# Performance work log

Measured on AMD Instinct MI355X. Metric: run time of the kernel, lower is better.

The kernel has to match this reference:

```python
import jax, jax.numpy as jnp
import numpy as np

C = 128          # hidden_channels
H = 8            # num_heads
D = C // H       # head dim = 16
OUT = 64         # out_channels
L = 2            # num_layers
NN = (30000, 60000, 6000)                 # poi, road, region node counts
NE = (200000, 300000, 200000, 100000)     # edges per edge type
ETS = ((0, 1), (1, 1), (1, 2), (2, 0))    # (src_type, dst_type) per edge type


def setup_inputs():
    key = jax.random.key(0)
    ks = iter(jax.random.split(key, 40))
    s = 1.0 / np.sqrt(C)
    sd = 1.0 / np.sqrt(D)
    inp = {}
    inp['x_poi'] = jax.random.normal(next(ks), (NN[0], C), jnp.float32)
    inp['x_road'] = jax.random.normal(next(ks), (NN[1], C), jnp.float32)
    inp['x_region'] = jax.random.normal(next(ks), (NN[2], C), jnp.float32)
    for et, (si, di) in enumerate(ETS):
        inp[f'e{et}_src'] = jax.random.randint(next(ks), (NE[et],), 0, NN[si], jnp.int32)
        inp[f'e{et}_dst'] = jax.random.randint(next(ks), (NE[et],), 0, NN[di], jnp.int32)
    # per-node-type input projection
    inp['lin_w'] = jax.random.normal(next(ks), (3, C, C), jnp.float32) * s
    inp['lin_b'] = jax.random.normal(next(ks), (3, C), jnp.float32) * 0.01
    # per-layer, per-node-type K/Q/V and output projections
    for nm in ('kw', 'qw', 'vw', 'aw'):
        inp[nm] = jax.random.normal(next(ks), (L, 3, C, C), jnp.float32) * s
    for nm in ('kb', 'qb', 'vb', 'ab'):
        inp[nm] = jax.random.normal(next(ks), (L, 3, C), jnp.float32) * 0.01
    # per-layer, per-edge-type relation matrices and priors
    inp['a_rel'] = jax.random.normal(next(ks), (L, 4, H, D, D), jnp.float32) * sd
    inp['m_rel'] = jax.random.normal(next(ks), (L, 4, H, D, D), jnp.float32) * sd
    inp['p_rel'] = jnp.ones((L, 4, H), jnp.float32)
    inp['skip'] = jnp.ones((L, 3), jnp.float32)
    inp['out_w'] = jax.random.normal(next(ks), (C, OUT), jnp.float32) * s
    inp['out_b'] = jnp.zeros((OUT,), jnp.float32)
    return inp


def _seg_softmax(alpha, dst, n):
    amax = jax.lax.stop_gradient(jax.ops.segment_max(alpha, dst, num_segments=n))
    ex = jnp.exp(alpha - amax[dst])
    den = jax.ops.segment_sum(ex, dst, num_segments=n)
    return ex / (den[dst] + 1e-16)


def _hgt_forward(xs, edges, lin_w, lin_b, kw, kb, qw, qb, vw, vb, aw, ab,
                 a_rel, m_rel, p_rel, skip, out_w, out_b):
    # per-node-type input linear + relu
    xs = [jax.nn.relu(xs[i] @ lin_w[i] + lin_b[i]) for i in range(3)]
    scale = 1.0 / np.sqrt(D)
    for l in range(L):
        k = [(xs[i] @ kw[l, i] + kb[l, i]).reshape(-1, H, D) for i in range(3)]
        q = [(xs[i] @ qw[l, i] + qb[l, i]).reshape(-1, H, D) for i in range(3)]
        v = [(xs[i] @ vw[l, i] + vb[l, i]).reshape(-1, H, D) for i in range(3)]
        agg = [jnp.zeros((NN[i], H, D), xs[i].dtype) for i in range(3)]
        for et, (si, di) in enumerate(ETS):
            src, dst = edges[et]
            n = NN[di]
            ke = jnp.einsum('ehd,hdf->ehf', k[si][src], a_rel[l, et])   # [E,H,D]
            alpha = jnp.einsum('ehd,ehd->eh', q[di][dst], ke) * p_rel[l, et] * scale
            alpha = _seg_softmax(alpha, dst, n)                          # [E,H]
            m = jnp.einsum('ehd,hdf->ehf', v[si][src], m_rel[l, et])    # [E,H,D]
            agg[di] = agg[di] + jax.ops.segment_sum(m * alpha[..., None], dst, num_segments=n)
        new_xs = []
        for i in range(3):
            o = jax.nn.gelu(agg[i].reshape(-1, C)) @ aw[l, i] + ab[l, i]
            beta = jax.nn.sigmoid(skip[l, i])
            o = beta * o + (1.0 - beta) * xs[i]
            new_xs.append(jax.nn.relu(o))  # HGT applies activation after each conv
        xs = new_xs
    return (xs[0] @ out_w + out_b, xs[1] @ out_w + out_b, xs[2] @ out_w + out_b)


def reference(x_poi, x_road, x_region,
              e0_src, e0_dst, e1_src, e1_dst, e2_src, e2_dst, e3_src, e3_dst,
              lin_w, lin_b, kw, kb, qw, qb, vw, vb, aw, ab,
              a_rel, m_rel, p_rel, skip, out_w, out_b):
    edges = ((e0_src, e0_dst), (e1_src, e1_dst), (e2_src, e2_dst), (e3_src, e3_dst))
    return _hgt_forward([x_poi, x_road, x_region], edges,
                        lin_w, lin_b, kw, kb, qw, qb, vw, vb, aw, ab,
                        a_rel, m_rel, p_rel, skip, out_w, out_b)
```

## Files before the change

### kernel.cpp

```cpp
#include <hip/hip_runtime.h>
#include <cstddef>
#include <cstdint>


typedef __attribute__((ext_vector_type(8))) short short8;
typedef __attribute__((ext_vector_type(4))) float floatx4;

__device__ __forceinline__ float gelu_fast(float x) {
    float u = 1.5957691216057308f * x * (1.0f + 0.044715f * x * x);
    return x / (1.0f + __expf(-u));
}

__device__ __forceinline__ unsigned short f2bf(float f) {
    unsigned u = __float_as_uint(f);
    u += 0x7fffu + ((u >> 16) & 1);
    return (unsigned short)(u >> 16);
}

__device__ __forceinline__ float bf2f(unsigned short h) {
    return __uint_as_float((unsigned)h << 16);
}

__device__ __forceinline__ void up8(uint4 u, float* f) {
    f[0] = __uint_as_float(u.x << 16); f[1] = __uint_as_float(u.x & 0xffff0000u);
    f[2] = __uint_as_float(u.y << 16); f[3] = __uint_as_float(u.y & 0xffff0000u);
    f[4] = __uint_as_float(u.z << 16); f[5] = __uint_as_float(u.z & 0xffff0000u);
    f[6] = __uint_as_float(u.w << 16); f[7] = __uint_as_float(u.w & 0xffff0000u);
}

__device__ __forceinline__ uint4 pk8(const float* f) {
    uint4 u;
    u.x = (unsigned)f2bf(f[0]) | ((unsigned)f2bf(f[1]) << 16);
    u.y = (unsigned)f2bf(f[2]) | ((unsigned)f2bf(f[3]) << 16);
    u.z = (unsigned)f2bf(f[4]) | ((unsigned)f2bf(f[5]) << 16);
    u.w = (unsigned)f2bf(f[6]) | ((unsigned)f2bf(f[7]) << 16);
    return u;
}

__global__ __launch_bounds__(256, 2) void gemm_proj_all(
    const unsigned short* __restrict__ xs_bf,
    const unsigned short* __restrict__ Wl,
    const float* __restrict__ bl,
    unsigned short* __restrict__ proj)
{
    const int    NN_[3]  = {30000, 60000, 6000};
    const int    NPAN[3] = {469, 938, 94};
    const int    OFFr[3] = {0, 30000, 90000};
    const int    WOFF[3] = {0, 49152, 131072};
    const int    BOFF[3] = {0, 384, 1024};
    const size_t POFF[3] = {0, 11520000u, 49920000u};
    const int    LDO[3]  = {384, 640, 384};

    int b = blockIdx.x, t, cp, rb;
    if (b < 590)      { t = 1; cp = b / 118; rb = b - cp * 118; }
    else if (b < 767) { int lb = b - 590; t = 0; cp = lb / 59; rb = lb - cp * 59; }
    else              { int lb = b - 767; t = 2; cp = lb / 12; rb = lb - cp * 12; }
    int p0 = rb * 8, p1 = p0 + 8;
    if (p1 > NPAN[t]) p1 = NPAN[t];

    const unsigned short* Abf = xs_bf + (size_t)OFFr[t] * 128;
    const unsigned short* Wt  = Wl + WOFF[t];
    const float* bias = bl + BOFF[t] + cp * 128;
    unsigned short* outbf = proj + POFF[t];
    const int ldo = LDO[t], Nrows = NN_[t];

    const int wave = threadIdx.x >> 6, lane = threadIdx.x & 63;
    const int quad = lane >> 4, l16 = lane & 15;

    short8 B[2][4][4];
    {
        const unsigned short* wb = Wt + (size_t)(cp * 128 + l16) * 128 + quad * 8;
        #pragma unroll
        for (int T = 0; T < 2; ++T)
            #pragma unroll
            for (int c = 0; c < 4; ++c)
                #pragma unroll
                for (int kc = 0; kc < 4; ++kc)
                    B[T][c][kc] = *(const short8*)(wb + (size_t)(T * 64 + c * 16) * 128 + kc * 32);
    }
    float4 bv[2][4];
    #pragma unroll
    for (int T = 0; T < 2; ++T)
        #pragma unroll
        for (int c = 0; c < 4; ++c)
            bv[T][c] = *(const float4*)(bias + T * 64 + c * 16 + quad * 4);

    short8 Acur[4];
    {
        int m = p0 * 64 + wave * 16 + l16; if (m >= Nrows) m = Nrows - 1;
        const unsigned short* ap = Abf + (size_t)m * 128 + quad * 8;
        #pragma unroll
        for (int kc = 0; kc < 4; ++kc) Acur[kc] = *(const short8*)(ap + kc * 32);
    }
    for (int p = p0; p < p1; ++p) {
        short8 Anx[4];
        {
            int m = (p + 1) * 64 + wave * 16 + l16; if (m >= Nrows) m = Nrows - 1;
            const unsigned short* ap = Abf + (size_t)m * 128 + quad * 8;
            #pragma unroll
            for (int kc = 0; kc < 4; ++kc) Anx[kc] = *(const short8*)(ap + kc * 32);
        }
        floatx4 acc[2][4];
        #pragma unroll
        for (int T = 0; T < 2; ++T)
            #pragma unroll
            for (int c = 0; c < 4; ++c) acc[T][c] = (floatx4){0.f, 0.f, 0.f, 0.f};
        #pragma unroll
        for (int kc = 0; kc < 4; ++kc)
            #pragma unroll
            for (int T = 0; T < 2; ++T)
                #pragma unroll
                for (int c = 0; c < 4; ++c)
                    acc[T][c] = __builtin_amdgcn_mfma_f32_16x16x32_bf16(B[T][c][kc], Acur[kc], acc[T][c], 0, 0, 0);
        int node = p * 64 + wave * 16 + l16;
        if (node < Nrows) {
            unsigned short* op = outbf + (size_t)node * ldo + cp * 128 + quad * 4;
            #pragma unroll
            for (int T = 0; T < 2; ++T)
                #pragma unroll
                for (int c = 0; c < 4; ++c) {
                    uint2 u;
                    u.x = (unsigned)f2bf(acc[T][c][0] + bv[T][c].x) |
                          ((unsigned)f2bf(acc[T][c][1] + bv[T][c].y) << 16);
                    u.y = (unsigned)f2bf(acc[T][c][2] + bv[T][c].z) |
                          ((unsigned)f2bf(acc[T][c][3] + bv[T][c].w) << 16);
                    *(uint2*)(op + T * 64 + c * 16) = u;
                }
        }
        #pragma unroll
        for (int kc = 0; kc < 4; ++kc) Acur[kc] = Anx[kc];
    }
}

template<bool AF32, bool GIN, bool SKIP>
__global__ __launch_bounds__(256, 2) void gemm_node(
    const void* __restrict__ a0v, const void* __restrict__ a1v, const void* __restrict__ a2v,
    const unsigned short* __restrict__ WtB, const float* __restrict__ biasB,
    const unsigned short* __restrict__ xoldB, const float* __restrict__ skipB,
    unsigned short* __restrict__ outB)
{
    const int TN[3]   = {30000, 60000, 6000};
    const int NPAN[3] = {469, 938, 94};
    const int TOFF[3] = {0, 30000, 90000};
    int b = blockIdx.x, t, rb;
    if (b < 235)      { t = 0; rb = b; }
    else if (b < 704) { t = 1; rb = b - 235; }
    else              { t = 2; rb = b - 704; }
    int p0 = rb * 2, p1 = p0 + 2;
    if (p1 > NPAN[t]) p1 = NPAN[t];
    int Nrows = TN[t];
    const void* av = (t == 0) ? a0v : (t == 1) ? a1v : a2v;
    const unsigned short* xold = xoldB + (size_t)TOFF[t] * 128;
    unsigned short* out = outB + (size_t)TOFF[t] * 128;

    const int wave = threadIdx.x >> 6, lane = threadIdx.x & 63;
    const int quad = lane >> 4, l16 = lane & 15;

    short8 B[8][4];
    {
        const unsigned short* wb = WtB + (size_t)t * 16384 + (size_t)l16 * 128 + quad * 8;
        #pragma unroll
        for (int c = 0; c < 8; ++c)
            #pragma unroll
            for (int kc = 0; kc < 4; ++kc)
                B[c][kc] = *(const short8*)(wb + (size_t)c * 2048 + kc * 32);
    }
    float beta = 0.f, omb = 0.f;
    if (SKIP) { beta = 1.0f / (1.0f + __expf(-skipB[t])); omb = 1.0f - beta; }

    short8 Acur[4];
    {
        int m = p0 * 64 + wave * 16 + l16; if (m >= Nrows) m = Nrows - 1;
        size_t base = (size_t)m * 128 + quad * 8;
        #pragma unroll
        for (int kc = 0; kc < 4; ++kc) {
            if (AF32) {
                const float* ap = (const float*)av + base;
                float4 f0 = *(const float4*)(ap + kc * 32);
                float4 f1 = *(const float4*)(ap + kc * 32 + 4);
                float af[8] = {f0.x, f0.y, f0.z, f0.w, f1.x, f1.y, f1.z, f1.w};
                short8 a;
                #pragma unroll
                for (int i = 0; i < 8; ++i) a[i] = (short)f2bf(af[i]);
                Acur[kc] = a;
            } else if (GIN) {
                const unsigned short* ap = (const unsigned short*)av + base;
                short8 a8 = *(const short8*)(ap + kc * 32);
                short8 a;
                #pragma unroll
                for (int i = 0; i < 8; ++i)
                    a[i] = (short)f2bf(gelu_fast(bf2f((unsigned short)a8[i])));
                Acur[kc] = a;
            } else {
                const unsigned short* ap = (const unsigned short*)av + base;
                Acur[kc] = *(const short8*)(ap + kc * 32);
            }
        }
    }
    for (int p = p0; p < p1; ++p) {
        float4 Fnx[4][2];
        short8 Snx[4];
        {
            int m = (p + 1) * 64 + wave * 16 + l16; if (m >= Nrows) m = Nrows - 1;
            size_t base = (size_t)m * 128 + quad * 8;
            #pragma unroll
            for (int kc = 0; kc < 4; ++kc) {
                if (AF32) {
                    const float* ap = (const float*)av + base;
                    Fnx[kc][0] = *(const float4*)(ap + kc * 32);
                    Fnx[kc][1] = *(const float4*)(ap + kc * 32 + 4);
                } else {
                    const unsigned short* ap = (const unsigned short*)av + base;
                    Snx[kc] = *(const short8*)(ap + kc * 32);
                }
            }
        }
        int node = p * 64 + wave * 16 + l16;
        int ncl = (node < Nrows) ? node : (Nrows - 1);
        uint2 xo[8];
        if (SKIP) {
            #pragma unroll
            for (int c = 0; c < 8; ++c)
                xo[c] = *(const uint2*)(xold + (size_t)ncl * 128 + c * 16 + quad * 4);
        }
        floatx4 acc[8];
        #pragma unroll
        for (int c = 0; c < 8; ++c) acc[c] = (floatx4){0.f, 0.f, 0.f, 0.f};
        #pragma unroll
        for (int kc = 0; kc < 4; ++kc)
            #pragma unroll
            for (int c = 0; c < 8; ++c)
                acc[c] = __builtin_amdgcn_mfma_f32_16x16x32_bf16(B[c][kc], Acur[kc], acc[c], 0, 0, 0);
        if (node < Nrows) {
            #pragma unroll
            for (int c = 0; c < 8; ++c) {
                int col0 = c * 16 + quad * 4;
                float4 bv = *(const float4*)(biasB + t * 128 + col0);
                float o0 = acc[c][0] + bv.x, o1 = acc[c][1] + bv.y;
                float o2 = acc[c][2] + bv.z, o3 = acc[c][3] + bv.w;
                if (SKIP) {
                    o0 = beta * o0 + omb * __uint_as_float(xo[c].x << 16);
                    o1 = beta * o1 + omb * __uint_as_float(xo[c].x & 0xffff0000u);
                    o2 = beta * o2 + omb * __uint_as_float(xo[c].y << 16);
                    o3 = beta * o3 + omb * __uint_as_float(xo[c].y & 0xffff0000u);
                }
                o0 = fmaxf(o0, 0.f); o1 = fmaxf(o1, 0.f);
                o2 = fmaxf(o2, 0.f); o3 = fmaxf(o3, 0.f);
                uint2 u;
                u.x = (unsigned)f2bf(o0) | ((unsigned)f2bf(o1) << 16);
                u.y = (unsigned)f2bf(o2) | ((unsigned)f2bf(o3) << 16);
                *(uint2*)(out + (size_t)node * 128 + col0) = u;
            }
        }
        #pragma unroll
        for (int kc = 0; kc < 4; ++kc) {
            if (AF32) {
                float af[8] = {Fnx[kc][0].x, Fnx[kc][0].y, Fnx[kc][0].z, Fnx[kc][0].w,
                               Fnx[kc][1].x, Fnx[kc][1].y, Fnx[kc][1].z, Fnx[kc][1].w};
                short8 a;
                #pragma unroll
                for (int i = 0; i < 8; ++i) a[i] = (short)f2bf(af[i]);
                Acur[kc] = a;
            } else if (GIN) {
                short8 a;
                #pragma unroll
                for (int i = 0; i < 8; ++i)
                    a[i] = (short)f2bf(gelu_fast(bf2f((unsigned short)Snx[kc][i])));
                Acur[kc] = a;
            } else {
                Acur[kc] = Snx[kc];
            }
        }
    }
}

__global__ __launch_bounds__(256, 3) void gemm_out(
    const unsigned short* __restrict__ Abf,
    const unsigned short* __restrict__ Wt,
    const float* __restrict__ bias,
    float* __restrict__ out, int Nrows)
{
    const int wave = threadIdx.x >> 6, lane = threadIdx.x & 63;
    const int quad = lane >> 4, l16 = lane & 15;
    int p0 = blockIdx.x * 4, p1 = p0 + 4;

    short8 B[4][4];
    {
        const unsigned short* wb = Wt + (size_t)l16 * 128 + quad * 8;
        #pragma unroll
        for (int c = 0; c < 4; ++c)
            #pragma unroll
            for (int kc = 0; kc < 4; ++kc)
                B[c][kc] = *(const short8*)(wb + (size_t)c * 2048 + kc * 32);
    }
    float4 bv[4];
    #pragma unroll
    for (int c = 0; c < 4; ++c) bv[c] = *(const float4*)(bias + c * 16 + quad * 4);

    short8 Acur[4];
    {
        int m = p0 * 64 + wave * 16 + l16; if (m >= Nrows) m = Nrows - 1;
        const unsigned short* ap = Abf + (size_t)m * 128 + quad * 8;
        #pragma unroll
        for (int kc = 0; kc < 4; ++kc) Acur[kc] = *(const short8*)(ap + kc * 32);
    }
    for (int p = p0; p < p1; ++p) {
        short8 Anx[4];
        {
            int m = (p + 1) * 64 + wave * 16 + l16; if (m >= Nrows) m = Nrows - 1;
            const unsigned short* ap = Abf + (size_t)m * 128 + quad * 8;
            #pragma unroll
            for (int kc = 0; kc < 4; ++kc) Anx[kc] = *(const short8*)(ap + kc * 32);
        }
        floatx4 acc[4];
        #pragma unroll
        for (int c = 0; c < 4; ++c) acc[c] = (floatx4){0.f, 0.f, 0.f, 0.f};
        #pragma unroll
        for (int kc = 0; kc < 4; ++kc)
            #pragma unroll
            for (int c = 0; c < 4; ++c)
                acc[c] = __builtin_amdgcn_mfma_f32_16x16x32_bf16(B[c][kc], Acur[kc], acc[c], 0, 0, 0);
        int node = p * 64 + wave * 16 + l16;
        if (node < Nrows) {
            #pragma unroll
            for (int c = 0; c < 4; ++c) {
                float4 o;
                o.x = acc[c][0] + bv[c].x; o.y = acc[c][1] + bv[c].y;
                o.z = acc[c][2] + bv[c].z; o.w = acc[c][3] + bv[c].w;
                *(float4*)(out + (size_t)node * 64 + c * 16 + quad * 4) = o;
            }
        }
        #pragma unroll
        for (int kc = 0; kc < 4; ++kc) Acur[kc] = Anx[kc];
    }
}

__global__ __launch_bounds__(128) void prep_qpack(
    const float* __restrict__ qw, const float* __restrict__ qb,
    unsigned short* __restrict__ Wpack, float* __restrict__ bpack)
{
    const int pre[3] = {0, 49152, 131072};
    const int preB[3] = {0, 384, 1024};
    int n = threadIdx.x, k = blockIdx.x, t = blockIdx.y, l = blockIdx.z;
    unsigned short* Wp = Wpack + (size_t)l * 180224 + pre[t];
    Wp[(size_t)n * 128 + k] = f2bf(qw[(size_t)(l * 3 + t) * 16384 + (size_t)k * 128 + n]);
    if (k == 0) bpack[l * 1408 + preB[t] + n] = qb[(l * 3 + t) * 128 + n];
}

__global__ __launch_bounds__(128) void fold_rel_pack(
    const float* __restrict__ kw, const float* __restrict__ kb,
    const float* __restrict__ vw, const float* __restrict__ vb,
    const float* __restrict__ a_rel, const float* __restrict__ m_rel,
    unsigned short* __restrict__ Wpack, float* __restrict__ bpack)
{
    const int SIv[4] = {0, 1, 1, 2};
    const int SLOT[4] = {0, 0, 1, 0};
    const int pre[3] = {0, 49152, 131072};
    const int preB[3] = {0, 384, 1024};
    int hf = threadIdx.x, h = hf >> 4, f = hf & 15;
    int c = blockIdx.x, et = blockIdx.y, l = blockIdx.z;
    int si = SIv[et];
    const float* kwp  = kw + (size_t)(l * 3 + si) * 16384;
    const float* vwp  = vw + (size_t)(l * 3 + si) * 16384;
    const float* kbp  = kb + (size_t)(l * 3 + si) * 128;
    const float* vbp  = vb + (size_t)(l * 3 + si) * 128;
    const float* arel = a_rel + (size_t)(l * 4 + et) * 2048;
    const float* mrel = m_rel + (size_t)(l * 4 + et) * 2048;
    float sk = 0.f, sv = 0.f;
    #pragma unroll
    for (int d = 0; d < 16; ++d) {
        float ar = arel[(h * 16 + d) * 16 + f];
        float mr = mrel[(h * 16 + d) * 16 + f];
        sk = fmaf(kwp[c * 128 + h * 16 + d], ar, sk);
        sv = fmaf(vwp[c * 128 + h * 16 + d], mr, sv);
    }
    int rowoff = 128 + 256 * SLOT[et];
    unsigned short* Wp = Wpack + (size_t)l * 180224 + pre[si];
    Wp[(size_t)(rowoff + hf) * 128 + c]       = f2bf(sk);
    Wp[(size_t)(rowoff + 128 + hf) * 128 + c] = f2bf(sv);
    if (c == 0) {
        float bk = 0.f, bvv = 0.f;
        #pragma unroll
        for (int d = 0; d < 16; ++d) {
            bk  = fmaf(kbp[h * 16 + d], arel[(h * 16 + d) * 16 + f], bk);
            bvv = fmaf(vbp[h * 16 + d], mrel[(h * 16 + d) * 16 + f], bvv);
        }
        float* bp = bpack + l * 1408 + preB[si];
        bp[rowoff + hf]       = bk;
        bp[rowoff + 128 + hf] = bvv;
    }
}

__global__ __launch_bounds__(128) void prep_w9(
    const float* __restrict__ lin_w, const float* __restrict__ aw,
    unsigned short* __restrict__ lwt, unsigned short* __restrict__ awt)
{
    int n = threadIdx.x, k = blockIdx.x, mi = blockIdx.y;
    const float* w; unsigned short* wt; int m;
    if (mi < 3) { w = lin_w; wt = lwt; m = mi; }
    else        { w = aw;    wt = awt; m = mi - 3; }
    wt[(size_t)m * 16384 + (size_t)n * 128 + k] =
        f2bf(w[(size_t)m * 16384 + (size_t)k * 128 + n]);
}

__global__ __launch_bounds__(64) void prep_owt(
    const float* __restrict__ ow, unsigned short* __restrict__ owt)
{
    int n = threadIdx.x, k = blockIdx.x;
    owt[(size_t)n * 128 + k] = f2bf(ow[(size_t)k * 64 + n]);
}

__global__ __launch_bounds__(256) void hist_all(
    const int* __restrict__ d0, const int* __restrict__ d1,
    const int* __restrict__ d2, const int* __restrict__ d3,
    int* __restrict__ deg4)
{
    const int Ev[4] = {200000, 300000, 200000, 100000};
    int et = blockIdx.y;
    int e = blockIdx.x * 256 + threadIdx.x;
    if (e >= Ev[et]) return;
    const int* d = et == 0 ? d0 : et == 1 ? d1 : et == 2 ? d2 : d3;
    atomicAdd(&deg4[et * 60000 + d[e]], 1);
}

__global__ __launch_bounds__(256) void scan_tile_all(
    const int* __restrict__ deg4,
    int* __restrict__ r0, int* __restrict__ r1, int* __restrict__ r2, int* __restrict__ r3,
    int* __restrict__ tsum4)
{
    const int Ndv[4] = {60000, 60000, 6000, 30000};
    __shared__ int ls[256];
    int et = blockIdx.y;
    int n = Ndv[et];
    const int* deg = deg4 + et * 60000;
    int* rowptr = et == 0 ? r0 : et == 1 ? r1 : et == 2 ? r2 : r3;
    int b = blockIdx.x, tid = threadIdx.x;
    int base = b * 1024 + tid * 4;
    int v0 = 0, v1 = 0, v2 = 0, v3 = 0;
    if (base + 3 < n) {
        int4 t = *(const int4*)(deg + base);
        v0 = t.x; v1 = t.y; v2 = t.z; v3 = t.w;
    } else {
        if (base + 0 < n) v0 = deg[base + 0];
        if (base + 1 < n) v1 = deg[base + 1];
        if (base + 2 < n) v2 = deg[base + 2];
        if (base + 3 < n) v3 = deg[base + 3];
    }
    int s = v0 + v1 + v2 + v3;
    ls[tid] = s;
    __syncthreads();
    #pragma unroll
    for (int off = 1; off < 256; off <<= 1) {
        int t = (tid >= off) ? ls[tid - off] : 0;
        __syncthreads();
        ls[tid] += t;
        __syncthreads();
    }
    int run = ls[tid] - s;
    int o0 = run; run += v0;
    int o1 = run; run += v1;
    int o2 = run; run += v2;
    int o3 = run;
    if (base + 3 < n) {
        *(int4*)(rowptr + base) = make_int4(o0, o1, o2, o3);
    } else {
        if (base + 0 < n) rowptr[base + 0] = o0;
        if (base + 1 < n) rowptr[base + 1] = o1;
        if (base + 2 < n) rowptr[base + 2] = o2;
    }
    if (tid == 255) tsum4[et * 64 + b] = ls[255];
}

__global__ __launch_bounds__(64) void scan_tsum_all(
    int* __restrict__ tsum4,
    int* __restrict__ r0, int* __restrict__ r1, int* __restrict__ r2, int* __restrict__ r3)
{
    const int Ndv[4] = {60000, 60000, 6000, 30000};
    int et = blockIdx.x;
    int n = Ndv[et];
    int nt = (n + 1023) >> 10;
    int* tileSum = tsum4 + et * 64;
    int* rowptr = et == 0 ? r0 : et == 1 ? r1 : et == 2 ? r2 : r3;
    int tid = threadIdx.x;
    int v = (tid < nt) ? tileSum[tid] : 0;
    int orig = v;
    #pragma unroll
    for (int off = 1; off < 64; off <<= 1) {
        int t = __shfl_up(v, off);
        if (tid >= off) v += t;
    }
    if (tid < nt) tileSum[tid] = v - orig;
    if (tid == nt - 1) rowptr[n] = v;
}

__global__ __launch_bounds__(256) void scan_add_all(
    int* __restrict__ r0, int* __restrict__ r1, int* __restrict__ r2, int* __restrict__ r3,
    const int* __restrict__ tsum4)
{
    const int Ndv[4] = {60000, 60000, 6000, 30000};
    int et = blockIdx.y;
    int n = Ndv[et];
    int* rowptr = et == 0 ? r0 : et == 1 ? r1 : et == 2 ? r2 : r3;
    int i = blockIdx.x * 256 + threadIdx.x;
    if (i < n) rowptr[i] += tsum4[et * 64 + (i >> 10)];
}

__global__ __launch_bounds__(256) void fill_all(
    const int* __restrict__ s0, const int* __restrict__ d0,
    const int* __restrict__ s1, const int* __restrict__ d1,
    const int* __restrict__ s2, const int* __restrict__ d2,
    const int* __restrict__ s3, const int* __restrict__ d3,
    const int* __restrict__ r0, const int* __restrict__ r1,
    const int* __restrict__ r2, const int* __restrict__ r3,
    int* __restrict__ deg4,
    int* __restrict__ c0, int* __restrict__ c1, int* __restrict__ c2, int* __restrict__ c3)
{
    const int Ev[4] = {200000, 300000, 200000, 100000};
    int et = blockIdx.y;
    int e = blockIdx.x * 256 + threadIdx.x;
    if (e >= Ev[et]) return;
    const int* src = et == 0 ? s0 : et == 1 ? s1 : et == 2 ? s2 : s3;
    const int* dst = et == 0 ? d0 : et == 1 ? d1 : et == 2 ? d2 : d3;
    const int* rowptr = et == 0 ? r0 : et == 1 ? r1 : et == 2 ? r2 : r3;
    int* csr = et == 0 ? c0 : et == 1 ? c1 : et == 2 ? c2 : c3;
    int d = dst[e];
    int pos = atomicAdd(&deg4[et * 60000 + d], 1);
    csr[rowptr[d] + pos] = src[e];
}

__device__ __forceinline__ int perm_key(
    const int* rp0, const int* rp1, const int* rp2, const int* rp3,
    int sec, int i)
{
    int d;
    if (sec == 0)      d = (rp0[i + 1] - rp0[i]) + (rp1[i + 1] - rp1[i]);
    else if (sec == 1) d = rp3[i + 1] - rp3[i];
    else               d = rp2[i + 1] - rp2[i];
    return d < 511 ? d : 511;
}

__global__ __launch_bounds__(256) void perm_hist(
    const int* __restrict__ rp0, const int* __restrict__ rp1,
    const int* __restrict__ rp2, const int* __restrict__ rp3,
    int* __restrict__ hist)
{
    const int N[3] = {60000, 30000, 6000};
    __shared__ int lh[512];
    int sec = blockIdx.y, tid = threadIdx.x;
    lh[tid] = 0; lh[tid + 256] = 0;
    __syncthreads();
    int i = blockIdx.x * 256 + tid;
    if (i < N[sec])
        atomicAdd(&lh[perm_key(rp0, rp1, rp2, rp3, sec, i)], 1);
    __syncthreads();
    if (lh[tid])       atomicAdd(&hist[sec * 512 + tid],       lh[tid]);
    if (lh[tid + 256]) atomicAdd(&hist[sec * 512 + tid + 256], lh[tid + 256]);
}

__global__ __launch_bounds__(512) void perm_scan(int* __restrict__ hist)
{
    __shared__ int ls[512];
    int* h = hist + blockIdx.x * 512;
    int tid = threadIdx.x;
    int v = h[tid];
    ls[tid] = v;
    __syncthreads();
    for (int off = 1; off < 512; off <<= 1) {
        int t = (tid >= off) ? ls[tid - off] : 0;
        __syncthreads();
        ls[tid] += t;
        __syncthreads();
    }
    h[tid] = ls[tid] - v;
}

__global__ __launch_bounds__(256) void perm_scatter(
    const int* __restrict__ rp0, const int* __restrict__ rp1,
    const int* __restrict__ rp2, const int* __restrict__ rp3,
    int* __restrict__ hist,
    int* __restrict__ permR, int* __restrict__ permP, int* __restrict__ permG)
{
    const int N[3] = {60000, 30000, 6000};
    __shared__ int lh[512];
    __shared__ int lofs[512];
    int sec = blockIdx.y, tid = threadIdx.x;
    lh[tid] = 0; lh[tid + 256] = 0;
    __syncthreads();
    int i = blockIdx.x * 256 + tid;
    int d = -1, lrank = 0;
    if (i < N[sec]) {
        d = perm_key(rp0, rp1, rp2, rp3, sec, i);
        lrank = atomicAdd(&lh[d], 1);
    }
    __syncthreads();
    if (lh[tid])       lofs[tid]       = atomicAdd(&hist[sec * 512 + tid],       lh[tid]);
    if (lh[tid + 256]) lofs[tid + 256] = atomicAdd(&hist[sec * 512 + tid + 256], lh[tid + 256]);
    __syncthreads();
    if (i < N[sec]) {
        int* perm = (sec == 0) ? permR : (sec == 1) ? permP : permG;
        perm[lofs[d] + lrank] = i;
    }
}

__device__ __forceinline__ void attn_edge(
    uint4 k0, uint4 k1, uint4 v0, uint4 v1,
    const float* qf, float ph, float& m, float& l, float* o)
{
    float kf[16];
    up8(k0, kf); up8(k1, kf + 8);
    float a = 0.f;
    #pragma unroll
    for (int i = 0; i < 16; ++i) a = fmaf(qf[i], kf[i], a);
    a *= ph;
    float d = a - m;
    if (d > 8.f) {
        float sc = __expf(-d);
        l *= sc;
        #pragma unroll
        for (int i = 0; i < 16; ++i) o[i] *= sc;
        m = a; d = 0.f;
    }
    float w = __expf(d);
    l += w;
    float vf[16];
    up8(v0, vf); up8(v1, vf + 8);
    #pragma unroll
    for (int i = 0; i < 16; ++i) o[i] = fmaf(w, vf[i], o[i]);
}

__device__ __forceinline__ void attn_run(
    const int* __restrict__ csr, int beg, int end,
    const unsigned short* __restrict__ kbase, int ld,
    const float* qf, float ph, float& m, float& l, float* o)
{
    int n = end - beg;
    if (n <= 0) return;
    const uint4* pA = (const uint4*)(kbase + (size_t)csr[beg] * ld);
    uint4 A0 = pA[0], A1 = pA[1], A2 = pA[16], A3 = pA[17];
    uint4 B0 = A0, B1 = A1, B2 = A2, B3 = A3;
    if (n > 1) {
        const uint4* pB = (const uint4*)(kbase + (size_t)csr[beg + 1] * ld);
        B0 = pB[0]; B1 = pB[1]; B2 = pB[16]; B3 = pB[17];
    }
    int j = beg;
    for (; j + 3 < end; j += 2) {
        const uint4* pC = (const uint4*)(kbase + (size_t)csr[j + 2] * ld);
        const uint4* pD = (const uint4*)(kbase + (size_t)csr[j + 3] * ld);
        uint4 C0 = pC[0], C1 = pC[1], C2 = pC[16], C3 = pC[17];
        uint4 D0 = pD[0], D1 = pD[1], D2 = pD[16], D3 = pD[17];
        float kf0[16], kf1[16];
        up8(A0, kf0); up8(A1, kf0 + 8);
        up8(B0, kf1); up8(B1, kf1 + 8);
        float a0 = 0.f, a1 = 0.f;
        #pragma unroll
        for (int i = 0; i < 16; ++i) {
            a0 = fmaf(qf[i], kf0[i], a0);
            a1 = fmaf(qf[i], kf1[i], a1);
        }
        a0 *= ph; a1 *= ph;
        float hi = fmaxf(a0, a1);
        float d = hi - m;
        if (d > 8.f) {
            float sc = __expf(-d);
            l *= sc;
            #pragma unroll
            for (int i = 0; i < 16; ++i) o[i] *= sc;
            m = hi;
        }
        float w0 = __expf(a0 - m), w1 = __expf(a1 - m);
        l += w0 + w1;
        float vf0[16], vf1[16];
        up8(A2, vf0); up8(A3, vf0 + 8);
        up8(B2, vf1); up8(B3, vf1 + 8);
        #pragma unroll
        for (int i = 0; i < 16; ++i)
            o[i] = fmaf(w1, vf1[i], fmaf(w0, vf0[i], o[i]));
        A0 = C0; A1 = C1; A2 = C2; A3 = C3;
        B0 = D0; B1 = D1; B2 = D2; B3 = D3;
    }
    int rem = end - j;
    attn_edge(A0, A1, A2, A3, qf, ph, m, l, o);
    if (rem >= 2) attn_edge(B0, B1, B2, B3, qf, ph, m, l, o);
    if (rem == 3) {
        const uint4* pC = (const uint4*)(kbase + (size_t)csr[j + 2] * ld);
        attn_edge(pC[0], pC[1], pC[16], pC[17], qf, ph, m, l, o);
    }
}

__global__ __launch_bounds__(256) void agg_all(
    const int* __restrict__ rp0, const int* __restrict__ cs0,
    const int* __restrict__ rp1, const int* __restrict__ cs1,
    const int* __restrict__ rp2, const int* __restrict__ cs2,
    const int* __restrict__ rp3, const int* __restrict__ cs3,
    const unsigned short* __restrict__ P0, const unsigned short* __restrict__ P1,
    const unsigned short* __restrict__ P2,
    const float* __restrict__ prl,
    const int* __restrict__ pmR, const int* __restrict__ pmP,
    const int* __restrict__ pmG,
    unsigned short* __restrict__ num)
{
    int gb = blockIdx.x, tid = threadIdx.x;
    float qf[16], o[16], r[16];
    if (gb < 1875) {
        int t = gb * 256 + tid;
        int node = pmR[t >> 3], h = t & 7;
        const uint4* qp = (const uint4*)(P1 + (size_t)node * 640 + h * 16);
        up8(qp[0], qf); up8(qp[1], qf + 8);
        float m0 = -INFINITY, l0 = 0.f;
        #pragma unroll
        for (int i = 0; i < 16; ++i) o[i] = 0.f;
        attn_run(cs0, rp0[node], rp0[node + 1], P0 + 128 + h * 16, 384,
                 qf, prl[h] * 0.25f, m0, l0, o);
        float i0 = 1.f / (l0 + 1e-16f);
        #pragma unroll
        for (int i = 0; i < 16; ++i) { r[i] = i0 * o[i]; o[i] = 0.f; }
        float m1 = -INFINITY, l1 = 0.f;
        attn_run(cs1, rp1[node], rp1[node + 1], P1 + 128 + h * 16, 640,
                 qf, prl[8 + h] * 0.25f, m1, l1, o);
        float i1 = 1.f / (l1 + 1e-16f);
        #pragma unroll
        for (int i = 0; i < 16; ++i) r[i] += i1 * o[i];
        uint4* np = (uint4*)(num + (size_t)(30000 + node) * 128 + h * 16);
        np[0] = pk8(r); np[1] = pk8(r + 8);
    } else if (gb < 2625) {
        int t = (gb - 1875) * 256 + tid;
        int node = pmG[t >> 5], h = t & 7, sub = (t >> 3) & 3;
        int beg0 = rp2[node], end0 = rp2[node + 1];
        int n = end0 - beg0;
        int beg = beg0 + ((n * sub) >> 2);
        int end = beg0 + ((n * (sub + 1)) >> 2);
        const uint4* qp = (const uint4*)(P2 + (size_t)node * 384 + h * 16);
        up8(qp[0], qf); up8(qp[1], qf + 8);
        float m = -INFINITY, l = 0.f;
        #pragma unroll
        for (int i = 0; i < 16; ++i) o[i] = 0.f;
        attn_run(cs2, beg, end, P1 + 384 + h * 16, 640,
                 qf, prl[16 + h] * 0.25f, m, l, o);
        #pragma unroll
        for (int st = 8; st <= 16; st <<= 1) {
            float mp = __shfl_xor(m, st);
            float lp = __shfl_xor(l, st);
            float mn = fmaxf(m, mp);
            float sc  = (l  > 0.f) ? __expf(m  - mn) : 0.f;
            float scp = (lp > 0.f) ? __expf(mp - mn) : 0.f;
            l = l * sc + lp * scp;
            #pragma unroll
            for (int i = 0; i < 16; ++i) {
                float op = __shfl_xor(o[i], st);
                o[i] = o[i] * sc + op * scp;
            }
            m = mn;
        }
        if (sub) return;
        float inv = 1.f / (l + 1e-16f);
        #pragma unroll
        for (int i = 0; i < 16; ++i) r[i] = inv * o[i];
        uint4* np = (uint4*)(num + (size_t)(90000 + node) * 128 + h * 16);
        np[0] = pk8(r); np[1] = pk8(r + 8);
    } else {
        int t = (gb - 2625) * 256 + tid;
        if (t >= 240000) return;
        int node = pmP[t >> 3], h = t & 7;
        const uint4* qp = (const uint4*)(P0 + (size_t)node * 384 + h * 16);
        up8(qp[0], qf); up8(qp[1], qf + 8);
        float m = -INFINITY, l = 0.f;
        #pragma unroll
        for (int i = 0; i < 16; ++i) o[i] = 0.f;
        attn_run(cs3, rp3[node], rp3[node + 1], P2 + 128 + h * 16, 384,
                 qf, prl[24 + h] * 0.25f, m, l, o);
        float inv = 1.f / (l + 1e-16f);
        #pragma unroll
        for (int i = 0; i < 16; ++i) r[i] = inv * o[i];
        uint4* np = (uint4*)(num + (size_t)node * 128 + h * 16);
        np[0] = pk8(r); np[1] = pk8(r + 8);
    }
}

extern "C" void kernel_launch(void* const* d_in, const int* in_sizes, int n_in,
                              void* d_out, int out_size, void* d_ws, size_t ws_size,
                              hipStream_t stream)
{
    (void)in_sizes; (void)n_in; (void)out_size; (void)ws_size;

    const float* xin[3] = {(const float*)d_in[0], (const float*)d_in[1], (const float*)d_in[2]};
    const int* esrc[4] = {(const int*)d_in[3], (const int*)d_in[5], (const int*)d_in[7], (const int*)d_in[9]};
    const int* edst[4] = {(const int*)d_in[4], (const int*)d_in[6], (const int*)d_in[8], (const int*)d_in[10]};
    const float* lin_w = (const float*)d_in[11];
    const float* lin_b = (const float*)d_in[12];
    const float* kw = (const float*)d_in[13];
    const float* qw = (const float*)d_in[14];
    const float* vw = (const float*)d_in[15];
    const float* aw = (const float*)d_in[16];
    const float* kb = (const float*)d_in[17];
    const float* qb = (const float*)d_in[18];
    const float* vb = (const float*)d_in[19];
    const float* ab = (const float*)d_in[20];
    const float* a_rel = (const float*)d_in[21];
    const float* m_rel = (const float*)d_in[22];
    const float* p_rel = (const float*)d_in[23];
    const float* skip  = (const float*)d_in[24];
    const float* out_w = (const float*)d_in[25];
    const float* out_b = (const float*)d_in[26];

    float* ws = (float*)d_ws;
    unsigned short* num   = (unsigned short*)ws;
    unsigned short* xs_bf = (unsigned short*)(ws + 6144000);
    unsigned short* proj  = (unsigned short*)(ws + 12288000);
    unsigned short* Wpack = (unsigned short*)(ws + 38400000);
    unsigned short* lwt   = (unsigned short*)(ws + 38580224);
    unsigned short* awt   = (unsigned short*)(ws + 38604800);
    unsigned short* owt   = (unsigned short*)(ws + 38653952);
    float*          bpack = ws + 38658048;
    int*            deg4  = (int*)(ws + 38660864);
    int*            tsum4 = (int*)(ws + 38900864);
    int* rp[4];
    rp[0] = (int*)(ws + 38901120);
    rp[1] = (int*)(ws + 38961128);
    rp[2] = (int*)(ws + 39021136);
    rp[3] = (int*)(ws + 39027144);
    int* cs[4];
    cs[0] = (int*)(ws + 39057152);
    cs[1] = (int*)(ws + 39257152);
    cs[2] = (int*)(ws + 39557152);
    cs[3] = (int*)(ws + 39757152);
    int* permR = deg4;
    int* permP = deg4 + 60000;
    int* permG = deg4 + 90000;
    int* phist = deg4 + 96000;

    unsigned short* P[3];
    P[0] = proj;
    P[1] = proj + (size_t)30000 * 384;
    P[2] = proj + (size_t)30000 * 384 + (size_t)60000 * 640;

    dim3 blk(256);

    hipMemsetAsync(deg4, 0, 960000, stream);
    hist_all<<<dim3(1172, 4), blk, 0, stream>>>(edst[0], edst[1], edst[2], edst[3], deg4);
    scan_tile_all<<<dim3(59, 4), blk, 0, stream>>>(deg4, rp[0], rp[1], rp[2], rp[3], tsum4);
    scan_tsum_all<<<dim3(4), dim3(64), 0, stream>>>(tsum4, rp[0], rp[1], rp[2], rp[3]);
    scan_add_all<<<dim3(235, 4), blk, 0, stream>>>(rp[0], rp[1], rp[2], rp[3], tsum4);
    hipMemsetAsync(deg4, 0, 960000, stream);
    fill_all<<<dim3(1172, 4), blk, 0, stream>>>(
        esrc[0], edst[0], esrc[1], edst[1], esrc[2], edst[2], esrc[3], edst[3],
        rp[0], rp[1], rp[2], rp[3], deg4, cs[0], cs[1], cs[2], cs[3]);

    hipMemsetAsync(phist, 0, 1536 * 4, stream);
    perm_hist<<<dim3(235, 3), blk, 0, stream>>>(rp[0], rp[1], rp[2], rp[3], phist);
    perm_scan<<<dim3(3), dim3(512), 0, stream>>>(phist);
    perm_scatter<<<dim3(235, 3), blk, 0, stream>>>(
        rp[0], rp[1], rp[2], rp[3], phist, permR, permP, permG);

    prep_qpack<<<dim3(128, 3, 2), dim3(128), 0, stream>>>(qw, qb, Wpack, bpack);
    fold_rel_pack<<<dim3(128, 4, 2), dim3(128), 0, stream>>>(
        kw, kb, vw, vb, a_rel, m_rel, Wpack, bpack);
    prep_w9<<<dim3(128, 9), dim3(128), 0, stream>>>(lin_w, aw, lwt, awt);
    prep_owt<<<dim3(128), dim3(64), 0, stream>>>(out_w, owt);

    gemm_node<true, false, false><<<dim3(751), blk, 0, stream>>>(
        xin[0], xin[1], xin[2], lwt, lin_b, nullptr, nullptr, xs_bf);

    for (int l = 0; l < 2; ++l) {
        gemm_proj_all<<<dim3(803), blk, 0, stream>>>(
            xs_bf, Wpack + (size_t)l * 180224, bpack + l * 1408, proj);

        agg_all<<<dim3(3563), blk, 0, stream>>>(
            rp[0], cs[0], rp[1], cs[1], rp[2], cs[2], rp[3], cs[3],
            P[0], P[1], P[2], p_rel + (size_t)l * 32,
            permR, permP, permG, num);

        gemm_node<false, true, true><<<dim3(751), blk, 0, stream>>>(
            num, num + (size_t)30000 * 128, num + (size_t)90000 * 128,
            awt + (size_t)l * 3 * 16384, ab + (size_t)l * 3 * 128,
            xs_bf, skip + l * 3, xs_bf);
    }

    gemm_out<<<dim3(375), blk, 0, stream>>>(
        xs_bf, owt, out_b, (float*)d_out, 96000);
}
```

Before: 589.9 us.

## Split road and POI attention edges across two lanes, fuse prep kernels

```diff
diff --git a/kernel.cpp b/kernel.cpp
--- a/kernel.cpp
+++ b/kernel.cpp
@@ -335,79 +335,74 @@
     }
 }
 
-__global__ __launch_bounds__(128) void prep_qpack(
+__global__ __launch_bounds__(128) void prep_all(
     const float* __restrict__ qw, const float* __restrict__ qb,
-    unsigned short* __restrict__ Wpack, float* __restrict__ bpack)
-{
-    const int pre[3] = {0, 49152, 131072};
-    const int preB[3] = {0, 384, 1024};
-    int n = threadIdx.x, k = blockIdx.x, t = blockIdx.y, l = blockIdx.z;
-    unsigned short* Wp = Wpack + (size_t)l * 180224 + pre[t];
-    Wp[(size_t)n * 128 + k] = f2bf(qw[(size_t)(l * 3 + t) * 16384 + (size_t)k * 128 + n]);
-    if (k == 0) bpack[l * 1408 + preB[t] + n] = qb[(l * 3 + t) * 128 + n];
-}
-
-__global__ __launch_bounds__(128) void fold_rel_pack(
     const float* __restrict__ kw, const float* __restrict__ kb,
     const float* __restrict__ vw, const float* __restrict__ vb,
     const float* __restrict__ a_rel, const float* __restrict__ m_rel,
-    unsigned short* __restrict__ Wpack, float* __restrict__ bpack)
-{
-    const int SIv[4] = {0, 1, 1, 2};
-    const int SLOT[4] = {0, 0, 1, 0};
+    const float* __restrict__ lin_w, const float* __restrict__ aw,
+    const float* __restrict__ ow,
+    unsigned short* __restrict__ Wpack, float* __restrict__ bpack,
+    unsigned short* __restrict__ lwt, unsigned short* __restrict__ awt,
+    unsigned short* __restrict__ owt)
+{
     const int pre[3] = {0, 49152, 131072};
     const int preB[3] = {0, 384, 1024};
-    int hf = threadIdx.x, h = hf >> 4, f = hf & 15;
-    int c = blockIdx.x, et = blockIdx.y, l = blockIdx.z;
-    int si = SIv[et];
-    const float* kwp  = kw + (size_t)(l * 3 + si) * 16384;
-    const float* vwp  = vw + (size_t)(l * 3 + si) * 16384;
-    const float* kbp  = kb + (size_t)(l * 3 + si) * 128;
-    const float* vbp  = vb + (size_t)(l * 3 + si) * 128;
-    const float* arel = a_rel + (size_t)(l * 4 + et) * 2048;
-    const float* mrel = m_rel + (size_t)(l * 4 + et) * 2048;
-    float sk = 0.f, sv = 0.f;
-    #pragma unroll
-    for (int d = 0; d < 16; ++d) {
-        float ar = arel[(h * 16 + d) * 16 + f];
-        float mr = mrel[(h * 16 + d) * 16 + f];
-        sk = fmaf(kwp[c * 128 + h * 16 + d], ar, sk);
-        sv = fmaf(vwp[c * 128 + h * 16 + d], mr, sv);
-    }
-    int rowoff = 128 + 256 * SLOT[et];
-    unsigned short* Wp = Wpack + (size_t)l * 180224 + pre[si];
-    Wp[(size_t)(rowoff + hf) * 128 + c]       = f2bf(sk);
-    Wp[(size_t)(rowoff + 128 + hf) * 128 + c] = f2bf(sv);
-    if (c == 0) {
-        float bk = 0.f, bvv = 0.f;
+    int b = blockIdx.x;
+    if (b < 768) {
+        int n = threadIdx.x;
+        int k = b & 127, r = b >> 7, t = r % 3, l = r / 3;
+        unsigned short* Wp = Wpack + (size_t)l * 180224 + pre[t];
+        Wp[(size_t)n * 128 + k] = f2bf(qw[(size_t)(l * 3 + t) * 16384 + (size_t)k * 128 + n]);
+        if (k == 0) bpack[l * 1408 + preB[t] + n] = qb[(l * 3 + t) * 128 + n];
+    } else if (b < 1792) {
+        const int SIv[4] = {0, 1, 1, 2};
+        const int SLOT[4] = {0, 0, 1, 0};
+        int bb = b - 768;
+        int hf = threadIdx.x, h = hf >> 4, f = hf & 15;
+        int c = bb & 127, et = (bb >> 7) & 3, l = bb >> 9;
+        int si = SIv[et];
+        const float* kwp  = kw + (size_t)(l * 3 + si) * 16384;
+        const float* vwp  = vw + (size_t)(l * 3 + si) * 16384;
+        const float* kbp  = kb + (size_t)(l * 3 + si) * 128;
+        const float* vbp  = vb + (size_t)(l * 3 + si) * 128;
+        const float* arel = a_rel + (size_t)(l * 4 + et) * 2048;
+        const float* mrel = m_rel + (size_t)(l * 4 + et) * 2048;
+        float sk = 0.f, sv = 0.f;
         #pragma unroll
         for (int d = 0; d < 16; ++d) {
-            bk  = fmaf(kbp[h * 16 + d], arel[(h * 16 + d) * 16 + f], bk);
-            bvv = fmaf(vbp[h * 16 + d], mrel[(h * 16 + d) * 16 + f], bvv);
-        }
-        float* bp = bpack + l * 1408 + preB[si];
-        bp[rowoff + hf]       = bk;
-        bp[rowoff + 128 + hf] = bvv;
-    }
-}
-
-__global__ __launch_bounds__(128) void prep_w9(
-    const float* __restrict__ lin_w, const float* __restrict__ aw,
-    unsigned short* __restrict__ lwt, unsigned short* __restrict__ awt)
-{
-    int n = threadIdx.x, k = blockIdx.x, mi = blockIdx.y;
-    const float* w; unsigned short* wt; int m;
-    if (mi < 3) { w = lin_w; wt = lwt; m = mi; }
-    else        { w = aw;    wt = awt; m = mi - 3; }
-    wt[(size_t)m * 16384 + (size_t)n * 128 + k] =
-        f2bf(w[(size_t)m * 16384 + (size_t)k * 128 + n]);
-}
-
-__global__ __launch_bounds__(64) void prep_owt(
-    const float* __restrict__ ow, unsigned short* __restrict__ owt)
-{
-    int n = threadIdx.x, k = blockIdx.x;
-    owt[(size_t)n * 128 + k] = f2bf(ow[(size_t)k * 64 + n]);
+            float ar = arel[(h * 16 + d) * 16 + f];
+            float mr = mrel[(h * 16 + d) * 16 + f];
+            sk = fmaf(kwp[c * 128 + h * 16 + d], ar, sk);
+            sv = fmaf(vwp[c * 128 + h * 16 + d], mr, sv);
+        }
+        int rowoff = 128 + 256 * SLOT[et];
+        unsigned short* Wp = Wpack + (size_t)l * 180224 + pre[si];
+        Wp[(size_t)(rowoff + hf) * 128 + c]       = f2bf(sk);
+        Wp[(size_t)(rowoff + 128 + hf) * 128 + c] = f2bf(sv);
+        if (c == 0) {
+            float bk = 0.f, bvv = 0.f;
+            #pragma unroll
+            for (int d = 0; d < 16; ++d) {
+                bk  = fmaf(kbp[h * 16 + d], arel[(h * 16 + d) * 16 + f], bk);
+                bvv = fmaf(vbp[h * 16 + d], mrel[(h * 16 + d) * 16 + f], bvv);
+            }
+            float* bp = bpack + l * 1408 + preB[si];
+            bp[rowoff + hf]       = bk;
+            bp[rowoff + 128 + hf] = bvv;
+        }
+    } else if (b < 2944) {
+        int bb = b - 1792;
+        int n = threadIdx.x, k = bb & 127, mi = bb >> 7;
+        const float* w; unsigned short* wt; int m;
+        if (mi < 3) { w = lin_w; wt = lwt; m = mi; }
+        else        { w = aw;    wt = awt; m = mi - 3; }
+        wt[(size_t)m * 16384 + (size_t)n * 128 + k] =
+            f2bf(w[(size_t)m * 16384 + (size_t)k * 128 + n]);
+    } else {
+        int k = b - 2944, n = threadIdx.x;
+        if (n < 64) owt[(size_t)n * 128 + k] = f2bf(ow[(size_t)k * 64 + n]);
+    }
 }
 
 __global__ __launch_bounds__(256) void hist_all(
@@ -687,6 +682,22 @@
     }
 }
 
+__device__ __forceinline__ void merge_sm(float& m, float& l, float* o, int st)
+{
+    float mp = __shfl_xor(m, st);
+    float lp = __shfl_xor(l, st);
+    float mn = fmaxf(m, mp);
+    float sc  = (l  > 0.f) ? __expf(m  - mn) : 0.f;
+    float scp = (lp > 0.f) ? __expf(mp - mn) : 0.f;
+    l = l * sc + lp * scp;
+    #pragma unroll
+    for (int i = 0; i < 16; ++i) {
+        float op = __shfl_xor(o[i], st);
+        o[i] = o[i] * sc + op * scp;
+    }
+    m = mn;
+}
+
 __global__ __launch_bounds__(256) void agg_all(
     const int* __restrict__ rp0, const int* __restrict__ cs0,
     const int* __restrict__ rp1, const int* __restrict__ cs1,
@@ -701,30 +712,37 @@
 {
     int gb = blockIdx.x, tid = threadIdx.x;
     float qf[16], o[16], r[16];
-    if (gb < 1875) {
+    if (gb < 3750) {
         int t = gb * 256 + tid;
-        int node = pmR[t >> 3], h = t & 7;
+        int node = pmR[59999 - (t >> 4)], h = t & 7, half = (t >> 3) & 1;
         const uint4* qp = (const uint4*)(P1 + (size_t)node * 640 + h * 16);
         up8(qp[0], qf); up8(qp[1], qf + 8);
+        int beg = rp0[node], end = rp0[node + 1], n = end - beg;
+        int b0 = beg + ((n * half) >> 1), e0 = beg + ((n * (half + 1)) >> 1);
         float m0 = -INFINITY, l0 = 0.f;
         #pragma unroll
         for (int i = 0; i < 16; ++i) o[i] = 0.f;
-        attn_run(cs0, rp0[node], rp0[node + 1], P0 + 128 + h * 16, 384,
+        attn_run(cs0, b0, e0, P0 + 128 + h * 16, 384,
                  qf, prl[h] * 0.25f, m0, l0, o);
+        merge_sm(m0, l0, o, 8);
         float i0 = 1.f / (l0 + 1e-16f);
         #pragma unroll
         for (int i = 0; i < 16; ++i) { r[i] = i0 * o[i]; o[i] = 0.f; }
+        beg = rp1[node]; end = rp1[node + 1]; n = end - beg;
+        b0 = beg + ((n * half) >> 1); e0 = beg + ((n * (half + 1)) >> 1);
         float m1 = -INFINITY, l1 = 0.f;
-        attn_run(cs1, rp1[node], rp1[node + 1], P1 + 128 + h * 16, 640,
+        attn_run(cs1, b0, e0, P1 + 128 + h * 16, 640,
                  qf, prl[8 + h] * 0.25f, m1, l1, o);
+        merge_sm(m1, l1, o, 8);
         float i1 = 1.f / (l1 + 1e-16f);
         #pragma unroll
         for (int i = 0; i < 16; ++i) r[i] += i1 * o[i];
+        if (half) return;
         uint4* np = (uint4*)(num + (size_t)(30000 + node) * 128 + h * 16);
         np[0] = pk8(r); np[1] = pk8(r + 8);
-    } else if (gb < 2625) {
-        int t = (gb - 1875) * 256 + tid;
-        int node = pmG[t >> 5], h = t & 7, sub = (t >> 3) & 3;
+    } else if (gb < 4500) {
+        int t = (gb - 3750) * 256 + tid;
+        int node = pmG[5999 - (t >> 5)], h = t & 7, sub = (t >> 3) & 3;
         int beg0 = rp2[node], end0 = rp2[node + 1];
         int n = end0 - beg0;
         int beg = beg0 + ((n * sub) >> 2);
@@ -736,21 +754,8 @@
         for (int i = 0; i < 16; ++i) o[i] = 0.f;
         attn_run(cs2, beg, end, P1 + 384 + h * 16, 640,
                  qf, prl[16 + h] * 0.25f, m, l, o);
-        #pragma unroll
-        for (int st = 8; st <= 16; st <<= 1) {
-            float mp = __shfl_xor(m, st);
-            float lp = __shfl_xor(l, st);
-            float mn = fmaxf(m, mp);
-            float sc  = (l  > 0.f) ? __expf(m  - mn) : 0.f;
-            float scp = (lp > 0.f) ? __expf(mp - mn) : 0.f;
-            l = l * sc + lp * scp;
-            #pragma unroll
-            for (int i = 0; i < 16; ++i) {
-                float op = __shfl_xor(o[i], st);
-                o[i] = o[i] * sc + op * scp;
-            }
-            m = mn;
-        }
+        merge_sm(m, l, o, 8);
+        merge_sm(m, l, o, 16);
         if (sub) return;
         float inv = 1.f / (l + 1e-16f);
         #pragma unroll
@@ -758,16 +763,19 @@
         uint4* np = (uint4*)(num + (size_t)(90000 + node) * 128 + h * 16);
         np[0] = pk8(r); np[1] = pk8(r + 8);
     } else {
-        int t = (gb - 2625) * 256 + tid;
-        if (t >= 240000) return;
-        int node = pmP[t >> 3], h = t & 7;
+        int t = (gb - 4500) * 256 + tid;
+        int node = pmP[29999 - (t >> 4)], h = t & 7, half = (t >> 3) & 1;
+        int beg = rp3[node], end = rp3[node + 1], n = end - beg;
+        int b0 = beg + ((n * half) >> 1), e0 = beg + ((n * (half + 1)) >> 1);
         const uint4* qp = (const uint4*)(P0 + (size_t)node * 384 + h * 16);
         up8(qp[0], qf); up8(qp[1], qf + 8);
         float m = -INFINITY, l = 0.f;
         #pragma unroll
         for (int i = 0; i < 16; ++i) o[i] = 0.f;
-        attn_run(cs3, rp3[node], rp3[node + 1], P2 + 128 + h * 16, 384,
+        attn_run(cs3, b0, e0, P2 + 128 + h * 16, 384,
                  qf, prl[24 + h] * 0.25f, m, l, o);
+        merge_sm(m, l, o, 8);
+        if (half) return;
         float inv = 1.f / (l + 1e-16f);
         #pragma unroll
         for (int i = 0; i < 16; ++i) r[i] = inv * o[i];
@@ -851,11 +859,9 @@
     perm_scatter<<<dim3(235, 3), blk, 0, stream>>>(
         rp[0], rp[1], rp[2], rp[3], phist, permR, permP, permG);
 
-    prep_qpack<<<dim3(128, 3, 2), dim3(128), 0, stream>>>(qw, qb, Wpack, bpack);
-    fold_rel_pack<<<dim3(128, 4, 2), dim3(128), 0, stream>>>(
-        kw, kb, vw, vb, a_rel, m_rel, Wpack, bpack);
-    prep_w9<<<dim3(128, 9), dim3(128), 0, stream>>>(lin_w, aw, lwt, awt);
-    prep_owt<<<dim3(128), dim3(64), 0, stream>>>(out_w, owt);
+    prep_all<<<dim3(3072), dim3(128), 0, stream>>>(
+        qw, qb, kw, kb, vw, vb, a_rel, m_rel, lin_w, aw, out_w,
+        Wpack, bpack, lwt, awt, owt);
 
     gemm_node<true, false, false><<<dim3(751), blk, 0, stream>>>(
         xin[0], xin[1], xin[2], lwt, lin_b, nullptr, nullptr, xs_bf);
@@ -864,7 +870,7 @@
         gemm_proj_all<<<dim3(803), blk, 0, stream>>>(
             xs_bf, Wpack + (size_t)l * 180224, bpack + l * 1408, proj);
 
-        agg_all<<<dim3(3563), blk, 0, stream>>>(
+        agg_all<<<dim3(6375), blk, 0, stream>>>(
             rp[0], cs[0], rp[1], cs[1], rp[2], cs[2], rp[3], cs[3],
             P[0], P[1], P[2], p_rel + (size_t)l * 32,
             permR, permP, permG, num);
```

Measured after the change: 599.8 us. Within noise of the previous version (+1.7%).
